# Kernel optimization log

Hardware: AMD Instinct MI355X
Metric: run time of the kernel (lower is better)

## Reference

```python
import jax, jax.numpy as jnp
from jax import lax
import numpy as np

T = 8
TAU = 2.0       # LIFNode tau
VTH = 1.0       # v_threshold for IF and LIF
ALPHA = 2.0     # surrogate.ATan default alpha
BN_EPS = 1e-5

# --- ATan surrogate-gradient heaviside (spikingjelly semantics) ---
@jax.custom_vjp
def heaviside_atan(x):
    return (x >= 0.0).astype(x.dtype)

def _h_fwd(x):
    return heaviside_atan(x), x

def _h_bwd(x, g):
    sg = (ALPHA / 2.0) / (1.0 + (jnp.pi / 2.0 * ALPHA * x) ** 2)
    return (g * sg,)

heaviside_atan.defvjp(_h_fwd, _h_bwd)

# --- multi-step IF node: v += x; spike; hard reset to 0 ---
def if_node(x_seq):
    def step(v, x):
        v = v + x
        s = heaviside_atan(v - VTH)
        return (1.0 - s) * v, s
    return lax.scan(step, jnp.zeros_like(x_seq[0]), x_seq)[1]

# --- multi-step LIF node (decay_input=True, v_reset=0, hard reset) ---
def lif_node(x_seq):
    def step(v, x):
        v = v + (x - v) / TAU
        s = heaviside_atan(v - VTH)
        return (1.0 - s) * v, s
    return lax.scan(step, jnp.zeros_like(x_seq[0]), x_seq)[1]

def conv2d(x, w, b):
    y = lax.conv_general_dilated(x, w, (1, 1), 'SAME', dimension_numbers=('NCHW', 'OIHW', 'NCHW'))
    return y + b[None, :, None, None]

def bn(x, g, b, m, v):
    scale = g * lax.rsqrt(v + BN_EPS)
    return (x - m[None, :, None, None]) * scale[None, :, None, None] + b[None, :, None, None]

def maxpool2(x):
    return lax.reduce_window(x, -jnp.inf, lax.max, (1, 1, 2, 2), (1, 1, 2, 2), 'VALID')


def setup_inputs():
    key = jax.random.key(0)
    ks = jax.random.split(key, 8)
    B = 32
    f32 = jnp.float32
    d = {}
    d['x'] = jax.random.normal(ks[0], (B, 1, 48, 48), f32)
    d['conv1_w'] = jax.random.normal(ks[1], (128, 1, 3, 3), f32) * 0.2
    d['conv1_b'] = jnp.zeros((128,), f32)
    d['bn1_g'] = jnp.ones((128,), f32)
    d['bn1_b'] = jnp.zeros((128,), f32)
    d['bn1_m'] = jnp.zeros((128,), f32)
    d['bn1_v'] = jnp.ones((128,), f32)
    d['conv2_w'] = jax.random.normal(ks[2], (128, 128, 3, 3), f32) * 0.03
    d['conv2_b'] = jnp.zeros((128,), f32)
    d['bn2_g'] = jnp.ones((128,), f32)
    d['bn2_b'] = jnp.zeros((128,), f32)
    d['bn2_m'] = jnp.zeros((128,), f32)
    d['bn2_v'] = jnp.ones((128,), f32)
    d['fc1_w'] = jax.random.normal(ks[3], (1152, 128 * 12 * 12), f32) * 0.007
    d['fc1_b'] = jnp.zeros((1152,), f32)
    d['fc2_w'] = jax.random.normal(ks[4], (128, 1152), f32) * 0.03
    d['fc2_b'] = jnp.zeros((128,), f32)
    d['fc3_w'] = jax.random.normal(ks[5], (7, 128), f32) * 0.09
    d['fc3_b'] = jnp.zeros((7,), f32)
    return d


def reference(x, conv1_w, conv1_b, bn1_g, bn1_b, bn1_m, bn1_v,
              conv2_w, conv2_b, bn2_g, bn2_b, bn2_m, bn2_v,
              fc1_w, fc1_b, fc2_w, fc2_b, fc3_w, fc3_b):
    B = x.shape[0]
    # layer1 (single-step): conv + BN (eval-mode), dropout is identity at eval
    h = bn(conv2d(x, conv1_w, conv1_b), bn1_g, bn1_b, bn1_m, bn1_v)  # [B,128,48,48]
    # repeat over T timesteps
    x_step = jnp.broadcast_to(h, (T,) + h.shape)                      # [T,B,128,48,48]
    # layer2: IF -> maxpool -> conv -> BN -> IF -> maxpool
    s1 = if_node(x_step)                                              # [T,B,128,48,48]
    p1 = maxpool2(s1.reshape((T * B,) + s1.shape[2:]))                # [T*B,128,24,24]
    c2 = bn(conv2d(p1, conv2_w, conv2_b), bn2_g, bn2_b, bn2_m, bn2_v)
    s2 = if_node(c2.reshape((T, B) + c2.shape[1:]))                   # [T,B,128,24,24]
    p2 = maxpool2(s2.reshape((T * B,) + s2.shape[2:]))                # [T*B,128,12,12]
    # layer3: flatten -> fc -> LIF -> fc -> LIF -> fc -> LIF
    f = p2.reshape(T, B, -1)                                          # [T,B,18432]
    l1 = lif_node(jnp.einsum('tbi,oi->tbo', f, fc1_w) + fc1_b)        # [T,B,1152]
    l2 = lif_node(jnp.einsum('tbi,oi->tbo', l1, fc2_w) + fc2_b)       # [T,B,128]
    l3 = lif_node(jnp.einsum('tbi,oi->tbo', l2, fc3_w) + fc3_b)       # [T,B,7]
    return l3.mean(axis=0)                                            # [B,7]
```

## Files before the change

### kernel.cpp

```cpp
#include <hip/hip_runtime.h>
#include <hip/hip_bf16.h>


typedef float  f32x4  __attribute__((ext_vector_type(4)));
typedef __bf16 bf16x8 __attribute__((ext_vector_type(8)));

#define T_STEPS 8

static const size_t OFF_P1    = 0;
static const size_t OFF_PART  = 0;
static const size_t OFF_WT    = 44302336;
static const size_t OFF_P2    = 45481984;
static const size_t OFF_W2T   = 54919168;
static const size_t OFF_L1S   = 55508992;

__device__ __forceinline__ unsigned short bf16_rne(float f) {
  unsigned u = __builtin_bit_cast(unsigned, f);
  u += 0x7FFFu + ((u >> 16) & 1u);
  return (unsigned short)(u >> 16);
}
__device__ __forceinline__ float bf16_to_f(unsigned short h) {
  unsigned u = ((unsigned)h) << 16;
  return __builtin_bit_cast(float, u);
}

__device__ __forceinline__ void split_pair(float f0, float f1, unsigned& hi, unsigned& lo) {
  __hip_bfloat162 h2 = __float22bfloat162_rn(make_float2(f0, f1));
  unsigned uh; __builtin_memcpy(&uh, &h2, 4);
  float g0 = __builtin_bit_cast(float, uh << 16);
  float g1 = __builtin_bit_cast(float, uh & 0xFFFF0000u);
  __hip_bfloat162 l2 = __float22bfloat162_rn(make_float2(f0 - g0, f1 - g1));
  unsigned ul; __builtin_memcpy(&ul, &l2, 4);
  hi = uh;
  lo = ul;
}

__device__ __forceinline__ void lds_load16(const void* g, void* l) {
  auto* gp = reinterpret_cast<const __attribute__((address_space(1))) unsigned int*>(
      reinterpret_cast<uintptr_t>(g));
  auto* lp = reinterpret_cast<__attribute__((address_space(3))) unsigned int*>(
      reinterpret_cast<uintptr_t>(l));
  __builtin_amdgcn_global_load_lds(gp, lp, 16, 0, 0);
}

__global__ __launch_bounds__(256) void prep_conv1(
    const float* __restrict__ conv2_w, const float* __restrict__ fc2_w,
    short* __restrict__ wt_hi, short* __restrict__ wt_lo,
    float* __restrict__ w2t, uint4* __restrict__ p1pad4,
    const float* __restrict__ x, const float* __restrict__ w1,
    const float* __restrict__ b1, const float* __restrict__ g1,
    const float* __restrict__ be1, const float* __restrict__ m1,
    const float* __restrict__ vv1, short* __restrict__ p1) {
  __shared__ float patch[2][16];
  const int blk = blockIdx.x;
  if (blk < 2752) {
    int i = blk * 256 + threadIdx.x;
    if (i < 147456) {
      int tap = i >> 14;
      int oc  = (i >> 7) & 127;
      int ic  = i & 127;
      float wv = conv2_w[oc * 1152 + ic * 9 + tap];
      unsigned short h = bf16_rne(wv);
      wt_hi[i] = (short)h;
      wt_lo[i] = (short)bf16_rne(wv - bf16_to_f(h));
    } else if (i < 294912) {
      int j = i - 147456;
      int o = j & 127, k = j >> 7;
      w2t[j] = fc2_w[o * 1152 + k];
    } else if (i < 704512) {
      int k = i - 294912;
      int tb = k / 1600;
      int rem = k - tb * 1600;
      int pos = rem >> 4, c8 = rem & 15;
      int y, xx;
      if (pos < 26)      { y = 0;  xx = pos; }
      else if (pos < 52) { y = 25; xx = pos - 26; }
      else { int jj = pos - 52; y = 1 + (jj >> 1); xx = (jj & 1) * 25; }
      p1pad4[(tb * 676 + y * 26 + xx) * 16 + c8] = make_uint4(0u, 0u, 0u, 0u);
    }
    return;
  }
  const int idx = blk - 2752;
  const int b = idx / 288;
  const int sp2 = idx - b * 288;
  const int half = threadIdx.x >> 7;
  const int c = threadIdx.x & 127;
  const int sp = sp2 * 2 + half;
  const int oy = sp / 24, ox = sp % 24;
  if (c < 16) {
    int py = c >> 2, px = c & 3;
    int iy = 2 * oy - 1 + py, ix = 2 * ox - 1 + px;
    float v = 0.f;
    if (iy >= 0 && iy < 48 && ix >= 0 && ix < 48) v = x[b * 2304 + iy * 48 + ix];
    patch[half][c] = v;
  }
  __syncthreads();
  float w[9];
#pragma unroll
  for (int i = 0; i < 9; ++i) w[i] = w1[c * 9 + i];
  float scale = g1[c] * rsqrtf(vv1[c] + 1e-5f);
  float shift = (b1[c] - m1[c]) * scale + be1[c];
  float h[4];
#pragma unroll
  for (int p = 0; p < 4; ++p) {
    int py = p >> 1, px = p & 1;
    float s = 0.f;
#pragma unroll
    for (int dy = 0; dy < 3; ++dy)
#pragma unroll
      for (int dx = 0; dx < 3; ++dx) s += patch[half][(py + dy) * 4 + (px + dx)] * w[dy * 3 + dx];
    h[p] = s * scale + shift;
  }
  float va = 0.f, vb = 0.f, vc = 0.f, vd = 0.f;
  size_t base = ((size_t)b * 676 + (size_t)(1 + oy) * 26 + (1 + ox)) * 128 + c;
#pragma unroll
  for (int t = 0; t < T_STEPS; ++t) {
    va += h[0]; vb += h[1]; vc += h[2]; vd += h[3];
    bool s0 = va >= 1.f, s1 = vb >= 1.f, s2 = vc >= 1.f, s3 = vd >= 1.f;
    p1[base + (size_t)t * (32 * 676 * 128)] = (s0 | s1 | s2 | s3) ? (short)0x3F80 : (short)0;
    if (s0) va = 0.f; if (s1) vb = 0.f; if (s2) vc = 0.f; if (s3) vd = 0.f;
  }
}

__global__ __launch_bounds__(256, 4) void conv2_gemm(
    const short* __restrict__ p1pad, const short* __restrict__ wt_hi, const short* __restrict__ wt_lo,
    const float* __restrict__ conv2_b, const float* __restrict__ bn2_g, const float* __restrict__ bn2_b,
    const float* __restrict__ bn2_m, const float* __restrict__ bn2_v, short* __restrict__ p2,
    int boff) {
  __shared__ __align__(16) short lds[12288];
  short* ldsA  = lds;
  short* ldsBh = lds + 4096;
  short* ldsBl = lds + 8192;

  const int tid = threadIdx.x;
  const int lane = tid & 63;
  const int w = tid >> 6;
  const int wm = w & 1, wn = w >> 1;
  const int b = boff + blockIdx.y;
  const int gy = blockIdx.x / 3;
  const int gx = blockIdx.x - gy * 3;

  const int cs = (lane & 3) ^ ((lane >> 3) & 3);
  int rowofsA[2], bofs[2];
#pragma unroll
  for (int j = 0; j < 2; ++j) {
    int r = j * 64 + w * 16 + (lane >> 2);
    int t = r >> 4, iy = (r >> 3) & 1, ix = r & 7;
    rowofsA[j] = (((t * 32 + b) * 676) + (2 * gy + iy) * 26 + (8 * gx + ix)) * 128 + cs * 8;
    bofs[j] = r * 128 + cs * 8;
  }

  f32x4 acc[4][4];
#pragma unroll
  for (int mi = 0; mi < 4; ++mi)
#pragma unroll
    for (int ni = 0; ni < 4; ++ni) acc[mi][ni] = (f32x4){0.f, 0.f, 0.f, 0.f};

#pragma unroll 1
  for (int s = 0; s < 36; ++s) {
    const int tap = s >> 2;
    const int kk = (s & 3) << 5;
    const int tapoff = ((tap / 3) * 26 + (tap % 3)) * 128;
    __syncthreads();
#pragma unroll
    for (int j = 0; j < 2; ++j) {
      lds_load16(p1pad + rowofsA[j] + tapoff + kk, ldsA + (j * 64 + w * 16) * 32 + lane * 8);
    }
    const int wtoff = tap * 16384 + kk;
#pragma unroll
    for (int j = 0; j < 2; ++j) {
      lds_load16(wt_hi + wtoff + bofs[j], ldsBh + (j * 64 + w * 16) * 32 + lane * 8);
      lds_load16(wt_lo + wtoff + bofs[j], ldsBl + (j * 64 + w * 16) * 32 + lane * 8);
    }
    __syncthreads();
    const int cch = lane >> 4;
    bf16x8 a[4], bh[4], bl[4];
#pragma unroll
    for (int i = 0; i < 4; ++i) {
      int r = wm * 64 + i * 16 + (lane & 15);
      a[i] = *(const bf16x8*)(ldsA + r * 32 + ((cch ^ ((r >> 1) & 3)) * 8));
      int n = wn * 64 + i * 16 + (lane & 15);
      bh[i] = *(const bf16x8*)(ldsBh + n * 32 + ((cch ^ ((n >> 1) & 3)) * 8));
      bl[i] = *(const bf16x8*)(ldsBl + n * 32 + ((cch ^ ((n >> 1) & 3)) * 8));
    }
#pragma unroll
    for (int mi = 0; mi < 4; ++mi)
#pragma unroll
      for (int ni = 0; ni < 4; ++ni) {
        acc[mi][ni] = __builtin_amdgcn_mfma_f32_16x16x32_bf16(a[mi], bh[ni], acc[mi][ni], 0, 0, 0);
        acc[mi][ni] = __builtin_amdgcn_mfma_f32_16x16x32_bf16(a[mi], bl[ni], acc[mi][ni], 0, 0, 0);
      }
  }

  float sc[4], sh[4];
#pragma unroll
  for (int ni = 0; ni < 4; ++ni) {
    int oc = wn * 64 + ni * 16 + (lane & 15);
    sc[ni] = bn2_g[oc] * rsqrtf(bn2_v[oc] + 1e-5f);
    sh[ni] = (conv2_b[oc] - bn2_m[oc]) * sc[ni] + bn2_b[oc];
  }
  float* ybuf = (float*)lds;
  const int S = 132;
  float v[16];
#pragma unroll
  for (int q = 0; q < 16; ++q) v[q] = 0.f;
  unsigned short* p2u = (unsigned short*)p2;
  __syncthreads();
#pragma unroll
  for (int q = 0; q < 4; ++q) {
    if (wm == (q >> 1)) {
#pragma unroll
      for (int ml = 0; ml < 2; ++ml) {
        const int mi = (q & 1) * 2 + ml;
#pragma unroll
        for (int ni = 0; ni < 4; ++ni)
#pragma unroll
          for (int r = 0; r < 4; ++r) {
            int lam = ml * 16 + ((lane >> 4) << 2) + r;
            int col = wn * 64 + ni * 16 + (lane & 15);
            ybuf[lam * S + col] = acc[mi][ni][r] * sc[ni] + sh[ni];
          }
      }
    }
    __syncthreads();
    if (tid < 128) {
      const int oc = tid;
#pragma unroll
      for (int tt = 0; tt < 2; ++tt) {
        int t = 2 * q + tt;
        unsigned short ov[4];
#pragma unroll
        for (int px = 0; px < 4; ++px) {
          bool any = false;
#pragma unroll
          for (int iy = 0; iy < 2; ++iy)
#pragma unroll
            for (int rx = 0; rx < 2; ++rx) {
              int pos = iy * 8 + 2 * px + rx;
              float xx = ybuf[(tt * 16 + pos) * S + oc];
              v[pos] += xx;
              bool ss = v[pos] >= 1.f;
              any |= ss;
              if (ss) v[pos] = 0.f;
            }
          ov[px] = any ? (unsigned short)0x3F80 : (unsigned short)0;
        }
        ushort4 o4; o4.x = ov[0]; o4.y = ov[1]; o4.z = ov[2]; o4.w = ov[3];
        *(ushort4*)(p2u + ((size_t)(t * 32 + b) * 128 + oc) * 144 + gy * 12 + gx * 4) = o4;
      }
    }
    __syncthreads();
  }
}

__global__ __launch_bounds__(512) void fc1_gemm(const short* __restrict__ p2,
                                                const float* __restrict__ fc1_w,
                                                float* __restrict__ part) {
  __shared__ __align__(16) short lds[32768];
  short* ldsA = lds;
  short* ldsBh = lds + 16384;
  short* ldsBl = lds + 24576;

  const int tid = threadIdx.x;
  const int lane = tid & 63;
  const int w = tid >> 6;
  const int wm = w & 3, wn = w >> 2;
  const int n0 = blockIdx.x * 128;
  const int kb = blockIdx.y * 576;

  const int g = (lane & 7) ^ (lane >> 3);
  int aofs[4];
#pragma unroll
  for (int j = 0; j < 4; ++j) {
    int r = w * 32 + j * 8 + (lane >> 3);
    aofs[j] = r * 18432 + g * 8;
  }
  const int bn = tid >> 2;
  const int c0 = (tid & 3) * 2;
  const float* wrow = fc1_w + (size_t)(n0 + bn) * 18432 + c0 * 8;
  const int bpos0 = (c0 ^ (bn & 7)) * 8;
  const int bpos1 = ((c0 + 1) ^ (bn & 7)) * 8;

  f32x4 acc[4][4];
#pragma unroll
  for (int mi = 0; mi < 4; ++mi)
#pragma unroll
    for (int ni = 0; ni < 4; ++ni) acc[mi][ni] = (f32x4){0.f, 0.f, 0.f, 0.f};

#pragma unroll 1
  for (int s = 0; s < 9; ++s) {
    const int koff = kb + s * 64;
    __syncthreads();
#pragma unroll
    for (int j = 0; j < 4; ++j) {
      lds_load16(p2 + aofs[j] + koff, ldsA + (w * 32 + j * 8) * 64 + lane * 8);
    }
    {
      const float4* wp = (const float4*)(wrow + koff);
      float4 q0 = wp[0], q1 = wp[1], q2 = wp[2], q3 = wp[3];
      unsigned h0, h1, h2, h3, h4, h5, h6, h7;
      unsigned l0, l1, l2, l3, l4, l5, l6, l7;
      split_pair(q0.x, q0.y, h0, l0);
      split_pair(q0.z, q0.w, h1, l1);
      split_pair(q1.x, q1.y, h2, l2);
      split_pair(q1.z, q1.w, h3, l3);
      split_pair(q2.x, q2.y, h4, l4);
      split_pair(q2.z, q2.w, h5, l5);
      split_pair(q3.x, q3.y, h6, l6);
      split_pair(q3.z, q3.w, h7, l7);
      uint4 H0; H0.x = h0; H0.y = h1; H0.z = h2; H0.w = h3;
      uint4 H1; H1.x = h4; H1.y = h5; H1.z = h6; H1.w = h7;
      uint4 L0; L0.x = l0; L0.y = l1; L0.z = l2; L0.w = l3;
      uint4 L1; L1.x = l4; L1.y = l5; L1.z = l6; L1.w = l7;
      *(uint4*)(ldsBh + bn * 64 + bpos0) = H0;
      *(uint4*)(ldsBh + bn * 64 + bpos1) = H1;
      *(uint4*)(ldsBl + bn * 64 + bpos0) = L0;
      *(uint4*)(ldsBl + bn * 64 + bpos1) = L1;
    }
    __syncthreads();
#pragma unroll
    for (int ks = 0; ks < 2; ++ks) {
      bf16x8 a[4], bh[4], bl[4];
      const int cch = ks * 4 + (lane >> 4);
#pragma unroll
      for (int i = 0; i < 4; ++i) {
        int r = wm * 64 + i * 16 + (lane & 15);
        a[i] = *(const bf16x8*)(ldsA + r * 64 + ((cch ^ (r & 7)) * 8));
        int n = wn * 64 + i * 16 + (lane & 15);
        bh[i] = *(const bf16x8*)(ldsBh + n * 64 + ((cch ^ (n & 7)) * 8));
        bl[i] = *(const bf16x8*)(ldsBl + n * 64 + ((cch ^ (n & 7)) * 8));
      }
#pragma unroll
      for (int mi = 0; mi < 4; ++mi)
#pragma unroll
        for (int ni = 0; ni < 4; ++ni) {
          acc[mi][ni] = __builtin_amdgcn_mfma_f32_16x16x32_bf16(a[mi], bh[ni], acc[mi][ni], 0, 0, 0);
          acc[mi][ni] = __builtin_amdgcn_mfma_f32_16x16x32_bf16(a[mi], bl[ni], acc[mi][ni], 0, 0, 0);
        }
    }
  }
  const size_t pbase = (size_t)(blockIdx.y * 9 + blockIdx.x) * 32768;
#pragma unroll
  for (int ni = 0; ni < 4; ++ni) {
    int j = wn * 64 + ni * 16 + (lane & 15);
#pragma unroll
    for (int mi = 0; mi < 4; ++mi) {
#pragma unroll
      for (int r = 0; r < 4; ++r) {
        int m = wm * 64 + mi * 16 + ((lane >> 4) << 2) + r;
        part[pbase + (size_t)m * 128 + j] = acc[mi][ni][r];
      }
    }
  }
}

__global__ __launch_bounds__(128) void fc1_reduce_lif(const float* __restrict__ part,
                                                      const float* __restrict__ fc1_b,
                                                      float* __restrict__ l1s) {
  int i = blockIdx.x * 128 + threadIdx.x;
  int b = i / 1152, n = i - b * 1152;
  int nt = n >> 7, j = n & 127;
  float bias = fc1_b[n];
  float v = 0.f;
#pragma unroll
  for (int t = 0; t < T_STEPS; ++t) {
    int m = t * 32 + b;
    float s = bias;
#pragma unroll 16
    for (int ks = 0; ks < 32; ++ks) s += part[(((size_t)ks * 9 + nt) * 256 + m) * 128 + j];
    v += (s - v) * 0.5f;
    bool sp = v >= 1.f;
    l1s[(size_t)m * 1152 + n] = sp ? 1.f : 0.f;
    if (sp) v = 0.f;
  }
}

__global__ __launch_bounds__(512) void tail(const float* __restrict__ l1s,
                                            const float* __restrict__ w2t,
                                            const float* __restrict__ b2,
                                            const float* __restrict__ w3,
                                            const float* __restrict__ b3,
                                            float* __restrict__ out) {
  __shared__ float sx[8][1152];
  __shared__ float part2[4][8][128];
  __shared__ float s2[8][128];
  __shared__ float y3[7][8];
  const int b = blockIdx.x;
  const int tid = threadIdx.x;
  for (int i = tid; i < 9216; i += 512) {
    int t = i / 1152, k = i - t * 1152;
    sx[t][k] = l1s[(size_t)(t * 32 + b) * 1152 + k];
  }
  __syncthreads();
  const int o = tid & 127, h = tid >> 7;
  float p[8];
#pragma unroll
  for (int t = 0; t < 8; ++t) p[t] = 0.f;
#pragma unroll 4
  for (int kk = 0; kk < 288; ++kk) {
    int k = h * 288 + kk;
    float wv = w2t[k * 128 + o];
#pragma unroll
    for (int t = 0; t < 8; ++t) p[t] += sx[t][k] * wv;
  }
#pragma unroll
  for (int t = 0; t < 8; ++t) part2[h][t][o] = p[t];
  __syncthreads();
  if (tid < 128) {
    float v = 0.f;
#pragma unroll
    for (int t = 0; t < 8; ++t) {
      float xx = part2[0][t][o] + part2[1][t][o] + part2[2][t][o] + part2[3][t][o] + b2[o];
      v += (xx - v) * 0.5f;
      bool s = v >= 1.f;
      s2[t][o] = s ? 1.f : 0.f;
      if (s) v = 0.f;
    }
  }
  __syncthreads();
  if (tid < 56) {
    int oo = tid >> 3, t = tid & 7;
    float d = 0.f;
    for (int k = 0; k < 128; ++k) d += s2[t][k] * w3[oo * 128 + k];
    y3[oo][t] = d + b3[oo];
  }
  __syncthreads();
  if (tid < 7) {
    float v = 0.f, a = 0.f;
#pragma unroll
    for (int t = 0; t < 8; ++t) {
      float xx = y3[tid][t];
      v += (xx - v) * 0.5f;
      bool s = v >= 1.f;
      a += s ? 1.f : 0.f;
      if (s) v = 0.f;
    }
    out[b * 7 + tid] = a * 0.125f;
  }
}

extern "C" void kernel_launch(void* const* d_in, const int* in_sizes, int n_in,
                              void* d_out, int out_size, void* d_ws, size_t ws_size,
                              hipStream_t stream) {
  const float* x       = (const float*)d_in[0];
  const float* conv1_w = (const float*)d_in[1];
  const float* conv1_b = (const float*)d_in[2];
  const float* bn1_g   = (const float*)d_in[3];
  const float* bn1_b   = (const float*)d_in[4];
  const float* bn1_m   = (const float*)d_in[5];
  const float* bn1_v   = (const float*)d_in[6];
  const float* conv2_w = (const float*)d_in[7];
  const float* conv2_b = (const float*)d_in[8];
  const float* bn2_g   = (const float*)d_in[9];
  const float* bn2_b   = (const float*)d_in[10];
  const float* bn2_m   = (const float*)d_in[11];
  const float* bn2_v   = (const float*)d_in[12];
  const float* fc1_w   = (const float*)d_in[13];
  const float* fc1_b   = (const float*)d_in[14];
  const float* fc2_w   = (const float*)d_in[15];
  const float* fc2_b   = (const float*)d_in[16];
  const float* fc3_w   = (const float*)d_in[17];
  const float* fc3_b   = (const float*)d_in[18];

  char* ws = (char*)d_ws;
  short* p1pad = (short*)(ws + OFF_P1);
  float* part  = (float*)(ws + OFF_PART);
  short* wt_hi = (short*)(ws + OFF_WT);
  short* wt_lo = wt_hi + 147456;
  short* p2    = (short*)(ws + OFF_P2);
  float* w2t   = (float*)(ws + OFF_W2T);
  float* l1s   = (float*)(ws + OFF_L1S);
  float* out   = (float*)d_out;

  prep_conv1<<<11968, 256, 0, stream>>>(conv2_w, fc2_w, wt_hi, wt_lo, w2t, (uint4*)p1pad,
                                        x, conv1_w, conv1_b, bn1_g, bn1_b, bn1_m, bn1_v, p1pad);
  conv2_gemm<<<dim3(36, 16), 256, 0, stream>>>(p1pad, wt_hi, wt_lo, conv2_b, bn2_g, bn2_b, bn2_m, bn2_v, p2, 0);
  conv2_gemm<<<dim3(36, 16), 256, 0, stream>>>(p1pad, wt_hi, wt_lo, conv2_b, bn2_g, bn2_b, bn2_m, bn2_v, p2, 16);
  fc1_gemm<<<dim3(9, 32), 512, 0, stream>>>(p2, fc1_w, part);
  fc1_reduce_lif<<<288, 128, 0, stream>>>(part, fc1_b, l1s);
  tail<<<32, 512, 0, stream>>>(l1s, w2t, fc2_b, fc3_w, fc3_b, out);
}
```

Before: 376.0 us.

## Retile fc1 GEMM to smaller 256x64 tiles with deeper split-K

Shrinks the fc1 GEMM block tile from 128 N columns with 512 threads to 64 columns with 256 threads, and doubles split-K from 32 to 64 slices of 288. The grid grows from 288 to 1152 blocks and LDS per block drops, so more blocks can be resident per CU and better hide the fp32 weight loads from HBM. In exchange the partial-sum buffer doubles, which means more write traffic and more reduction work in fc1_reduce_lif (64 slices instead of 32). The activation (A) tile is now reloaded by twice as many N-blocks, and the workspace offsets are shifted to fit the larger buffer.

```diff
diff --git a/kernel.cpp b/kernel.cpp
--- a/kernel.cpp
+++ b/kernel.cpp
@@ -9,10 +9,10 @@
 
 static const size_t OFF_P1    = 0;
 static const size_t OFF_PART  = 0;
-static const size_t OFF_WT    = 44302336;
-static const size_t OFF_P2    = 45481984;
-static const size_t OFF_W2T   = 54919168;
-static const size_t OFF_L1S   = 55508992;
+static const size_t OFF_WT    = 75497472;
+static const size_t OFF_P2    = 76677120;
+static const size_t OFF_W2T   = 86114304;
+static const size_t OFF_L1S   = 86704128;
 
 __device__ __forceinline__ unsigned short bf16_rne(float f) {
   unsigned u = __builtin_bit_cast(unsigned, f);
@@ -253,33 +253,31 @@
   }
 }
 
-__global__ __launch_bounds__(512) void fc1_gemm(const short* __restrict__ p2,
-                                                const float* __restrict__ fc1_w,
-                                                float* __restrict__ part) {
-  __shared__ __align__(16) short lds[32768];
+__global__ __launch_bounds__(256, 4) void fc1_gemm(const short* __restrict__ p2,
+                                                   const float* __restrict__ fc1_w,
+                                                   float* __restrict__ part) {
+  __shared__ __align__(16) short lds[12288];
   short* ldsA = lds;
-  short* ldsBh = lds + 16384;
-  short* ldsBl = lds + 24576;
+  short* ldsBh = lds + 8192;
+  short* ldsBl = lds + 10240;
 
   const int tid = threadIdx.x;
   const int lane = tid & 63;
   const int w = tid >> 6;
-  const int wm = w & 3, wn = w >> 2;
-  const int n0 = blockIdx.x * 128;
-  const int kb = blockIdx.y * 576;
-
-  const int g = (lane & 7) ^ (lane >> 3);
+  const int n0 = blockIdx.x * 64;
+  const int kb = blockIdx.y * 288;
+
+  const int cs = (lane & 3) ^ ((lane >> 3) & 3);
   int aofs[4];
 #pragma unroll
   for (int j = 0; j < 4; ++j) {
-    int r = w * 32 + j * 8 + (lane >> 3);
-    aofs[j] = r * 18432 + g * 8;
+    int r = j * 64 + w * 16 + (lane >> 2);
+    aofs[j] = r * 18432 + cs * 8;
   }
   const int bn = tid >> 2;
-  const int c0 = (tid & 3) * 2;
+  const int c0 = tid & 3;
   const float* wrow = fc1_w + (size_t)(n0 + bn) * 18432 + c0 * 8;
-  const int bpos0 = (c0 ^ (bn & 7)) * 8;
-  const int bpos1 = ((c0 + 1) ^ (bn & 7)) * 8;
+  const int bslot = (c0 ^ ((bn >> 1) & 3)) * 8;
 
   f32x4 acc[4][4];
 #pragma unroll
@@ -289,66 +287,54 @@
 
 #pragma unroll 1
   for (int s = 0; s < 9; ++s) {
-    const int koff = kb + s * 64;
+    const int koff = kb + s * 32;
     __syncthreads();
 #pragma unroll
     for (int j = 0; j < 4; ++j) {
-      lds_load16(p2 + aofs[j] + koff, ldsA + (w * 32 + j * 8) * 64 + lane * 8);
+      lds_load16(p2 + aofs[j] + koff, ldsA + (j * 64 + w * 16) * 32 + lane * 8);
     }
     {
       const float4* wp = (const float4*)(wrow + koff);
-      float4 q0 = wp[0], q1 = wp[1], q2 = wp[2], q3 = wp[3];
-      unsigned h0, h1, h2, h3, h4, h5, h6, h7;
-      unsigned l0, l1, l2, l3, l4, l5, l6, l7;
+      float4 q0 = wp[0], q1 = wp[1];
+      unsigned h0, h1, h2, h3, l0, l1, l2, l3;
       split_pair(q0.x, q0.y, h0, l0);
       split_pair(q0.z, q0.w, h1, l1);
       split_pair(q1.x, q1.y, h2, l2);
       split_pair(q1.z, q1.w, h3, l3);
-      split_pair(q2.x, q2.y, h4, l4);
-      split_pair(q2.z, q2.w, h5, l5);
-      split_pair(q3.x, q3.y, h6, l6);
-      split_pair(q3.z, q3.w, h7, l7);
-      uint4 H0; H0.x = h0; H0.y = h1; H0.z = h2; H0.w = h3;
-      uint4 H1; H1.x = h4; H1.y = h5; H1.z = h6; H1.w = h7;
-      uint4 L0; L0.x = l0; L0.y = l1; L0.z = l2; L0.w = l3;
-      uint4 L1; L1.x = l4; L1.y = l5; L1.z = l6; L1.w = l7;
-      *(uint4*)(ldsBh + bn * 64 + bpos0) = H0;
-      *(uint4*)(ldsBh + bn * 64 + bpos1) = H1;
-      *(uint4*)(ldsBl + bn * 64 + bpos0) = L0;
-      *(uint4*)(ldsBl + bn * 64 + bpos1) = L1;
-    }
-    __syncthreads();
-#pragma unroll
-    for (int ks = 0; ks < 2; ++ks) {
-      bf16x8 a[4], bh[4], bl[4];
-      const int cch = ks * 4 + (lane >> 4);
-#pragma unroll
-      for (int i = 0; i < 4; ++i) {
-        int r = wm * 64 + i * 16 + (lane & 15);
-        a[i] = *(const bf16x8*)(ldsA + r * 64 + ((cch ^ (r & 7)) * 8));
-        int n = wn * 64 + i * 16 + (lane & 15);
-        bh[i] = *(const bf16x8*)(ldsBh + n * 64 + ((cch ^ (n & 7)) * 8));
-        bl[i] = *(const bf16x8*)(ldsBl + n * 64 + ((cch ^ (n & 7)) * 8));
+      uint4 H; H.x = h0; H.y = h1; H.z = h2; H.w = h3;
+      uint4 L; L.x = l0; L.y = l1; L.z = l2; L.w = l3;
+      *(uint4*)(ldsBh + bn * 32 + bslot) = H;
+      *(uint4*)(ldsBl + bn * 32 + bslot) = L;
+    }
+    __syncthreads();
+    const int cch = lane >> 4;
+    bf16x8 a[4], bh[4], bl[4];
+#pragma unroll
+    for (int i = 0; i < 4; ++i) {
+      int r = w * 64 + i * 16 + (lane & 15);
+      a[i] = *(const bf16x8*)(ldsA + r * 32 + ((cch ^ ((r >> 1) & 3)) * 8));
+      int n = i * 16 + (lane & 15);
+      bh[i] = *(const bf16x8*)(ldsBh + n * 32 + ((cch ^ ((n >> 1) & 3)) * 8));
+      bl[i] = *(const bf16x8*)(ldsBl + n * 32 + ((cch ^ ((n >> 1) & 3)) * 8));
+    }
+#pragma unroll
+    for (int mi = 0; mi < 4; ++mi)
+#pragma unroll
+      for (int ni = 0; ni < 4; ++ni) {
+        acc[mi][ni] = __builtin_amdgcn_mfma_f32_16x16x32_bf16(a[mi], bh[ni], acc[mi][ni], 0, 0, 0);
+        acc[mi][ni] = __builtin_amdgcn_mfma_f32_16x16x32_bf16(a[mi], bl[ni], acc[mi][ni], 0, 0, 0);
       }
-#pragma unroll
-      for (int mi = 0; mi < 4; ++mi)
-#pragma unroll
-        for (int ni = 0; ni < 4; ++ni) {
-          acc[mi][ni] = __builtin_amdgcn_mfma_f32_16x16x32_bf16(a[mi], bh[ni], acc[mi][ni], 0, 0, 0);
-          acc[mi][ni] = __builtin_amdgcn_mfma_f32_16x16x32_bf16(a[mi], bl[ni], acc[mi][ni], 0, 0, 0);
-        }
-    }
-  }
-  const size_t pbase = (size_t)(blockIdx.y * 9 + blockIdx.x) * 32768;
+  }
+  float* pb = part + (size_t)(blockIdx.y * 18 + blockIdx.x) * 16384;
 #pragma unroll
   for (int ni = 0; ni < 4; ++ni) {
-    int j = wn * 64 + ni * 16 + (lane & 15);
+    int j = ni * 16 + (lane & 15);
 #pragma unroll
     for (int mi = 0; mi < 4; ++mi) {
 #pragma unroll
       for (int r = 0; r < 4; ++r) {
-        int m = wm * 64 + mi * 16 + ((lane >> 4) << 2) + r;
-        part[pbase + (size_t)m * 128 + j] = acc[mi][ni][r];
+        int m = w * 64 + mi * 16 + ((lane >> 4) << 2) + r;
+        pb[m * 64 + j] = acc[mi][ni][r];
       }
     }
   }
@@ -359,7 +345,7 @@
                                                       float* __restrict__ l1s) {
   int i = blockIdx.x * 128 + threadIdx.x;
   int b = i / 1152, n = i - b * 1152;
-  int nt = n >> 7, j = n & 127;
+  int nt = n >> 6, j = n & 63;
   float bias = fc1_b[n];
   float v = 0.f;
 #pragma unroll
@@ -367,7 +353,7 @@
     int m = t * 32 + b;
     float s = bias;
 #pragma unroll 16
-    for (int ks = 0; ks < 32; ++ks) s += part[(((size_t)ks * 9 + nt) * 256 + m) * 128 + j];
+    for (int ks = 0; ks < 64; ++ks) s += part[(((size_t)ks * 18 + nt) * 256 + m) * 64 + j];
     v += (s - v) * 0.5f;
     bool sp = v >= 1.f;
     l1s[(size_t)m * 1152 + n] = sp ? 1.f : 0.f;
@@ -476,7 +462,7 @@
                                         x, conv1_w, conv1_b, bn1_g, bn1_b, bn1_m, bn1_v, p1pad);
   conv2_gemm<<<dim3(36, 16), 256, 0, stream>>>(p1pad, wt_hi, wt_lo, conv2_b, bn2_g, bn2_b, bn2_m, bn2_v, p2, 0);
   conv2_gemm<<<dim3(36, 16), 256, 0, stream>>>(p1pad, wt_hi, wt_lo, conv2_b, bn2_g, bn2_b, bn2_m, bn2_v, p2, 16);
-  fc1_gemm<<<dim3(9, 32), 512, 0, stream>>>(p2, fc1_w, part);
+  fc1_gemm<<<dim3(18, 64), 256, 0, stream>>>(p2, fc1_w, part);
   fc1_reduce_lif<<<288, 128, 0, stream>>>(part, fc1_b, l1s);
   tail<<<32, 512, 0, stream>>>(l1s, w2t, fc2_b, fc3_w, fc3_b, out);
 }
```

Measured after the change: 386.6 us. +2.8%, slower.
